# Kernel optimization log

Measured on AMD Instinct MI355X. Metric: run time of the kernel, lower is better.

## Reference

```python
import jax, jax.numpy as jnp
import numpy as np

WIN = 9
WIN_SIZE = float(WIN ** 3)
LBD = 1.0
EPS = 1e-5


def _box_sum(x, win=WIN):
    """Separable sum over a win^3 window with zero padding == conv3d with all-ones kernel."""
    pad = win // 2
    for ax in (2, 3, 4):  # spatial axes of [N, C, H, W, D]
        wd = [1] * 5
        wd[ax] = win
        padc = [(0, 0)] * 5
        padc[ax] = (pad, pad)
        x = jax.lax.reduce_window(x, 0.0, jax.lax.add, tuple(wd), (1, 1, 1, 1, 1), padc)
    return x


def _warp3d(images, flows):
    """Trilinear warp. images [B,G,C,H,W,D], flows [B,G,3,H,W,D] (voxel displacements,
    channels ordered as (H, W, D) axes). Border-clamped sampling."""
    B, G, C, H, W, D = images.shape
    N = B * G
    img = images.reshape(N, C, H, W, D)
    flo = flows.reshape(N, 3, H, W, D)
    ft = flo.dtype
    gh = jnp.arange(H, dtype=ft).reshape(H, 1, 1)
    gw = jnp.arange(W, dtype=ft).reshape(1, W, 1)
    gd = jnp.arange(D, dtype=ft).reshape(1, 1, D)
    ch = jnp.clip(flo[:, 0] + gh, 0.0, H - 1.0)
    cw = jnp.clip(flo[:, 1] + gw, 0.0, W - 1.0)
    cd = jnp.clip(flo[:, 2] + gd, 0.0, D - 1.0)
    h0f = jnp.floor(ch); w0f = jnp.floor(cw); d0f = jnp.floor(cd)
    fh = ch - h0f; fw = cw - w0f; fd = cd - d0f
    h0 = h0f.astype(jnp.int32); w0 = w0f.astype(jnp.int32); d0 = d0f.astype(jnp.int32)
    h1 = jnp.minimum(h0 + 1, H - 1)
    w1 = jnp.minimum(w0 + 1, W - 1)
    d1 = jnp.minimum(d0 + 1, D - 1)
    flat = img.reshape(N, C, H * W * D)

    def gather(hi, wi, di):
        lin = ((hi * W + wi) * D + di).reshape(N, 1, H * W * D)
        return jnp.take_along_axis(flat, lin, axis=2).reshape(N, C, H, W, D)

    out = jnp.zeros_like(img)
    for hi, wh in ((h0, 1.0 - fh), (h1, fh)):
        for wi, ww in ((w0, 1.0 - fw), (w1, fw)):
            for di, wdw in ((d0, 1.0 - fd), (d1, fd)):
                w8 = (wh * ww * wdw)[:, None]  # [N,1,H,W,D]
                out = out + w8 * gather(hi, wi, di)
    return out.reshape(B, G, C, H, W, D)


def setup_inputs() -> dict:
    key = jax.random.key(0)
    k1, k2 = jax.random.split(key)
    images = jax.random.normal(k1, (1, 4, 1, 128, 128, 128), dtype=jnp.float32)
    warps = jax.random.normal(k2, (1, 4, 3, 128, 128, 128), dtype=jnp.float32)
    return {"images": images, "warps": warps}


def reference(images, warps):
    B, G, C, H, W, D = images.shape
    warped = _warp3d(images, warps).reshape(B * G, C, H, W, D)
    # groupwise template = mean over the B*G warped volumes, broadcast back
    template = jnp.broadcast_to(jnp.mean(warped, axis=0, keepdims=True), warped.shape)
    Ii, Ji = template, warped
    # 5 stat channels: I, J, I^2, J^2, IJ; groups=5 box-filter conv == per-channel box sum
    stats = jnp.concatenate([Ii, Ji, Ii * Ii, Ji * Ji, Ii * Ji], axis=1)
    sums = _box_sum(stats)
    I_sum, J_sum, I2_sum, J2_sum, IJ_sum = jnp.split(sums, 5, axis=1)
    cross = IJ_sum - J_sum / WIN_SIZE * I_sum
    I_var = I2_sum - I_sum / WIN_SIZE * I_sum
    J_var = J2_sum - J_sum / WIN_SIZE * J_sum
    cc = cross * cross / (I_var * J_var + EPS)
    lncc = -jnp.mean(cc)
    # Grad3d('l2') on warps [B,G,3,H,W,D]: dx over H (axis 3), dy over W (axis 4), dz over D (axis 5)
    dx = jnp.square(warps[:, :, :, 1:] - warps[:, :, :, :-1])
    dy = jnp.square(warps[:, :, :, :, 1:] - warps[:, :, :, :, :-1])
    dz = jnp.square(warps[..., 1:] - warps[..., :-1])
    g2 = (jnp.mean(dx) + jnp.mean(dy) + jnp.mean(dz)) / 3.0
    return lncc + LBD * g2
```

## Files before the change

### kernel.cpp

```cpp
#include <hip/hip_runtime.h>
#include <hip/hip_bf16.h>


#define NVOX (128*128*128)
#define NGRP 4
#define NCH 14

__global__ __launch_bounds__(256) void k_pack(const float* __restrict__ img,
                                              float4* __restrict__ P4)
{
    int idx = blockIdx.x * 256 + threadIdx.x;
    int v = idx & (NVOX - 1);
    int g = idx >> 21;
    int d = v & 127;
    int w = (v >> 7) & 127;
    const float* im = img + (size_t)g * NVOX;
    int vd1 = (d < 127) ? v + 1 : v;
    int vw1 = (w < 127) ? v + 128 : v;
    int vw1d1 = (d < 127) ? vw1 + 1 : vw1;
    P4[idx] = make_float4(im[v], im[vd1], im[vw1], im[vw1d1]);
}

__global__ __launch_bounds__(256) void k_warp_stats_p4(
    const float4* __restrict__ P4, const float* __restrict__ flo,
    float* __restrict__ S, double* __restrict__ pg2)
{
    __shared__ float jt[NGRP][256];
    int t = threadIdx.x;
    int v = blockIdx.x * 256 + t;
    int d = v & 127;
    int w = (v >> 7) & 127;
    int h = v >> 14;
    float g2s = 0.f;

#pragma unroll
    for (int g = 0; g < NGRP; ++g) {
        const float* f = flo + (size_t)g * 3 * NVOX;
        float fx = f[v], fy = f[NVOX + v], fz = f[2 * NVOX + v];
        if (h < 127) {
            float a = f[v + 16384] - fx;
            float b = f[NVOX + v + 16384] - fy;
            float c = f[2 * NVOX + v + 16384] - fz;
            g2s += a * a + b * b + c * c;
        }
        if (w < 127) {
            float a = f[v + 128] - fx;
            float b = f[NVOX + v + 128] - fy;
            float c = f[2 * NVOX + v + 128] - fz;
            g2s += a * a + b * b + c * c;
        }
        if (d < 127) {
            float a = f[v + 1] - fx;
            float b = f[NVOX + v + 1] - fy;
            float c = f[2 * NVOX + v + 1] - fz;
            g2s += a * a + b * b + c * c;
        }
        float ch = fminf(fmaxf(fx + (float)h, 0.f), 127.f);
        float cw = fminf(fmaxf(fy + (float)w, 0.f), 127.f);
        float cd = fminf(fmaxf(fz + (float)d, 0.f), 127.f);
        float h0f = floorf(ch), w0f = floorf(cw), d0f = floorf(cd);
        int h0 = (int)h0f, w0 = (int)w0f, d0 = (int)d0f;
        float fh = ch - h0f, fw = cw - w0f, fd = cd - d0f;
        int h1 = min(h0 + 1, 127);
        const float4* P = P4 + (size_t)g * NVOX;
        float4 q0 = P[h0 * 16384 + w0 * 128 + d0];
        float4 q1 = P[h1 * 16384 + w0 * 128 + d0];
        float c00 = q0.x + fd * (q0.y - q0.x);
        float c01 = q0.z + fd * (q0.w - q0.z);
        float c10 = q1.x + fd * (q1.y - q1.x);
        float c11 = q1.z + fd * (q1.w - q1.z);
        float c0 = c00 + fw * (c01 - c00);
        float c1 = c10 + fw * (c11 - c10);
        jt[g][t] = c0 + fh * (c1 - c0);
    }
    __syncthreads();

    float s[NCH];
#pragma unroll
    for (int c = 0; c < NCH; ++c) s[c] = 0.f;
    int lbase = t & 128;
#pragma unroll
    for (int k = -4; k <= 4; ++k) {
        int q = d + k;
        if ((unsigned)q < 128u) {
            int tq = lbase + q;
            float j0 = jt[0][tq], j1 = jt[1][tq], j2 = jt[2][tq], j3 = jt[3][tq];
            float tm = 0.25f * (j0 + j1 + j2 + j3);
            s[0] += tm;       s[1] += tm * tm;
            s[2] += j0;  s[3] += j0 * j0;  s[4]  += tm * j0;
            s[5] += j1;  s[6] += j1 * j1;  s[7]  += tm * j1;
            s[8] += j2;  s[9] += j2 * j2;  s[10] += tm * j2;
            s[11] += j3; s[12] += j3 * j3; s[13] += tm * j3;
        }
    }
#pragma unroll
    for (int c = 0; c < NCH; ++c) S[(size_t)c * NVOX + v] = s[c];

    double val = (double)g2s;
    for (int off = 32; off; off >>= 1) val += __shfl_down(val, off, 64);
    __shared__ double wsum[4];
    int lane = t & 63, wid = t >> 6;
    if (lane == 0) wsum[wid] = val;
    __syncthreads();
    if (t == 0) pg2[blockIdx.x] = wsum[0] + wsum[1] + wsum[2] + wsum[3];
}

__global__ __launch_bounds__(256) void k_warp_stats_direct(
    const float* __restrict__ img, const float* __restrict__ flo,
    float* __restrict__ S, double* __restrict__ pg2)
{
    __shared__ float jt[NGRP][256];
    int t = threadIdx.x;
    int v = blockIdx.x * 256 + t;
    int d = v & 127;
    int w = (v >> 7) & 127;
    int h = v >> 14;
    float g2s = 0.f;

#pragma unroll
    for (int g = 0; g < NGRP; ++g) {
        const float* f = flo + (size_t)g * 3 * NVOX;
        float fx = f[v], fy = f[NVOX + v], fz = f[2 * NVOX + v];
        if (h < 127) {
            float a = f[v + 16384] - fx;
            float b = f[NVOX + v + 16384] - fy;
            float c = f[2 * NVOX + v + 16384] - fz;
            g2s += a * a + b * b + c * c;
        }
        if (w < 127) {
            float a = f[v + 128] - fx;
            float b = f[NVOX + v + 128] - fy;
            float c = f[2 * NVOX + v + 128] - fz;
            g2s += a * a + b * b + c * c;
        }
        if (d < 127) {
            float a = f[v + 1] - fx;
            float b = f[NVOX + v + 1] - fy;
            float c = f[2 * NVOX + v + 1] - fz;
            g2s += a * a + b * b + c * c;
        }
        float ch = fminf(fmaxf(fx + (float)h, 0.f), 127.f);
        float cw = fminf(fmaxf(fy + (float)w, 0.f), 127.f);
        float cd = fminf(fmaxf(fz + (float)d, 0.f), 127.f);
        float h0f = floorf(ch), w0f = floorf(cw), d0f = floorf(cd);
        int h0 = (int)h0f, w0 = (int)w0f, d0 = (int)d0f;
        float fh = ch - h0f, fw = cw - w0f, fd = cd - d0f;
        int h1 = min(h0 + 1, 127), w1 = min(w0 + 1, 127), d1 = min(d0 + 1, 127);
        const float* im = img + (size_t)g * NVOX;
        int b00 = (h0 * 128 + w0) * 128;
        int b01 = (h0 * 128 + w1) * 128;
        int b10 = (h1 * 128 + w0) * 128;
        int b11 = (h1 * 128 + w1) * 128;
        float v000 = im[b00 + d0], v001 = im[b00 + d1];
        float v010 = im[b01 + d0], v011 = im[b01 + d1];
        float v100 = im[b10 + d0], v101 = im[b10 + d1];
        float v110 = im[b11 + d0], v111 = im[b11 + d1];
        float c00 = v000 + fd * (v001 - v000);
        float c01 = v010 + fd * (v011 - v010);
        float c10 = v100 + fd * (v101 - v100);
        float c11 = v110 + fd * (v111 - v110);
        float c0 = c00 + fw * (c01 - c00);
        float c1 = c10 + fw * (c11 - c10);
        jt[g][t] = c0 + fh * (c1 - c0);
    }
    __syncthreads();

    float s[NCH];
#pragma unroll
    for (int c = 0; c < NCH; ++c) s[c] = 0.f;
    int lbase = t & 128;
#pragma unroll
    for (int k = -4; k <= 4; ++k) {
        int q = d + k;
        if ((unsigned)q < 128u) {
            int tq = lbase + q;
            float j0 = jt[0][tq], j1 = jt[1][tq], j2 = jt[2][tq], j3 = jt[3][tq];
            float tm = 0.25f * (j0 + j1 + j2 + j3);
            s[0] += tm;       s[1] += tm * tm;
            s[2] += j0;  s[3] += j0 * j0;  s[4]  += tm * j0;
            s[5] += j1;  s[6] += j1 * j1;  s[7]  += tm * j1;
            s[8] += j2;  s[9] += j2 * j2;  s[10] += tm * j2;
            s[11] += j3; s[12] += j3 * j3; s[13] += tm * j3;
        }
    }
#pragma unroll
    for (int c = 0; c < NCH; ++c) S[(size_t)c * NVOX + v] = s[c];

    double val = (double)g2s;
    for (int off = 32; off; off >>= 1) val += __shfl_down(val, off, 64);
    __shared__ double wsum[4];
    int lane = t & 63, wid = t >> 6;
    if (lane == 0) wsum[wid] = val;
    __syncthreads();
    if (t == 0) pg2[blockIdx.x] = wsum[0] + wsum[1] + wsum[2] + wsum[3];
}

__global__ __launch_bounds__(256) void k_sum_w(float* __restrict__ S)
{
    __shared__ float tile[128 * 64];
    int t = threadIdx.x;
    int bid = blockIdx.x;
    int half = bid & 1;
    int chh = bid >> 1;
    size_t base = (size_t)chh * 16384 + half * 64;
#pragma unroll
    for (int it = 0; it < 8; ++it) {
        int idx4 = it * 256 + t;
        int w = idx4 >> 4, dq = idx4 & 15;
        *(float4*)(tile + w * 64 + dq * 4) =
            *(const float4*)(S + base + (size_t)w * 128 + dq * 4);
    }
    __syncthreads();
    int dq = t & 15;
    int wq = t >> 4;
    int w0 = wq * 8;
    float4 s = make_float4(0.f, 0.f, 0.f, 0.f);
#pragma unroll
    for (int k = -4; k <= 4; ++k) {
        int q = w0 + k;
        if ((unsigned)q < 128u) {
            float4 tv = *(const float4*)(tile + q * 64 + dq * 4);
            s.x += tv.x; s.y += tv.y; s.z += tv.z; s.w += tv.w;
        }
    }
    *(float4*)(S + base + (size_t)w0 * 128 + dq * 4) = s;
#pragma unroll
    for (int wi = 1; wi < 8; ++wi) {
        int w = w0 + wi;
        int qa = w + 4;
        if (qa < 128) {
            float4 tv = *(const float4*)(tile + qa * 64 + dq * 4);
            s.x += tv.x; s.y += tv.y; s.z += tv.z; s.w += tv.w;
        }
        int qr = w - 5;
        if (qr >= 0) {
            float4 tv = *(const float4*)(tile + qr * 64 + dq * 4);
            s.x -= tv.x; s.y -= tv.y; s.z -= tv.z; s.w -= tv.w;
        }
        *(float4*)(S + base + (size_t)w * 128 + dq * 4) = s;
    }
}

__device__ __forceinline__ float cc4(float4 I, float4 I2, float4 J, float4 J2, float4 IJ)
{
    const float inv = 1.0f / 729.0f;
    float r = 0.f;
    {
        float cr = IJ.x - J.x * I.x * inv, iv = I2.x - I.x * I.x * inv, jv = J2.x - J.x * J.x * inv;
        r += cr * cr / (iv * jv + 1e-5f);
    }
    {
        float cr = IJ.y - J.y * I.y * inv, iv = I2.y - I.y * I.y * inv, jv = J2.y - J.y * J.y * inv;
        r += cr * cr / (iv * jv + 1e-5f);
    }
    {
        float cr = IJ.z - J.z * I.z * inv, iv = I2.z - I.z * I.z * inv, jv = J2.z - J.z * J.z * inv;
        r += cr * cr / (iv * jv + 1e-5f);
    }
    {
        float cr = IJ.w - J.w * I.w * inv, iv = I2.w - I.w * I.w * inv, jv = J2.w - J.w * J.w * inv;
        r += cr * cr / (iv * jv + 1e-5f);
    }
    return r;
}

#define LOADH(c, a0, a1)                                                       \
    do {                                                                       \
        const float* cp = S + (size_t)(c) * NVOX + cbase;                      \
        _Pragma("unroll")                                                      \
        for (int it = 0; it < 3; ++it) {                                       \
            int idx = it * 256 + t;                                            \
            if (idx < 640) {                           \
                int row = idx >> 4, dqu = idx & 15;                            \
                int rr = r0 + row;                                             \
                float4 vv = make_float4(0.f, 0.f, 0.f, 0.f);                   \
                if ((unsigned)rr < 128u)                                       \
                    vv = *(const float4*)(cp + (size_t)rr * 16384 + dqu * 4);  \
                int la = row * 65 + dqu * 4;                                   \
                tile[la] = vv.x; tile[la + 1] = vv.y;                          \
                tile[la + 2] = vv.z; tile[la + 3] = vv.w;                      \
            }                                                                  \
        }                                                                      \
        __syncthreads();                                                       \
        {                                                                      \
            int hl = hg * 2;                                                   \
            float4 sum = make_float4(0.f, 0.f, 0.f, 0.f);                      \
            _Pragma("unroll")                                                  \
            for (int k = 0; k < 9; ++k) {                                      \
                const float* tp = tile + (hl + k) * 65 + dq * 4;               \
                sum.x += tp[0]; sum.y += tp[1]; sum.z += tp[2]; sum.w += tp[3];\
            }                                                                  \
            a0 = sum;                                                          \
            const float* ta = tile + (hl + 9) * 65 + dq * 4;                   \
            const float* tr = tile + hl * 65 + dq * 4;                         \
            sum.x += ta[0] - tr[0]; sum.y += ta[1] - tr[1];                    \
            sum.z += ta[2] - tr[2]; sum.w += ta[3] - tr[3];                    \
            a1 = sum;                                                          \
        }                                                                      \
        __syncthreads();                                                       \
    } while (0)

__global__ __launch_bounds__(256) void k_sum_h_cc(const float* __restrict__ S,
                                                  double* __restrict__ pcc)
{
    __shared__ float tile[40 * 65];
    int t = threadIdx.x;
    int bid = blockIdx.x;
    int dh = bid & 1;
    int hq = (bid >> 1) & 3;
    int w = bid >> 3;
    int r0 = hq * 32 - 4;
    size_t cbase = (size_t)w * 128 + dh * 64;
    int dq = t & 15;
    int hg = t >> 4;

    float4 Ia0, Ia1, I2a0, I2a1, Ja0, Ja1, J2a0, J2a1, IJa0, IJa1;
    float lsum = 0.f;

    LOADH(0, Ia0, Ia1);
    LOADH(1, I2a0, I2a1);
    for (int g = 0; g < NGRP; ++g) {
        LOADH(2 + 3 * g, Ja0, Ja1);
        LOADH(3 + 3 * g, J2a0, J2a1);
        LOADH(4 + 3 * g, IJa0, IJa1);
        lsum += cc4(Ia0, I2a0, Ja0, J2a0, IJa0);
        lsum += cc4(Ia1, I2a1, Ja1, J2a1, IJa1);
    }

    double val = (double)lsum;
    for (int off = 32; off; off >>= 1) val += __shfl_down(val, off, 64);
    __shared__ double wsum[4];
    int lane = t & 63, wid = t >> 6;
    if (lane == 0) wsum[wid] = val;
    __syncthreads();
    if (t == 0) pcc[bid] = wsum[0] + wsum[1] + wsum[2] + wsum[3];
}

__global__ __launch_bounds__(256) void k_finalize(const double* __restrict__ pg2,
                                                  const double* __restrict__ pcc,
                                                  float* __restrict__ out)
{
    double s_cc = 0.0, s_g2 = 0.0;
    for (int i = threadIdx.x; i < 1024; i += 256) s_cc += pcc[i];
    for (int i = threadIdx.x; i < 8192; i += 256) s_g2 += pg2[i];
    for (int off = 32; off; off >>= 1) {
        s_cc += __shfl_down(s_cc, off, 64);
        s_g2 += __shfl_down(s_g2, off, 64);
    }
    __shared__ double a[4], b[4];
    int lane = threadIdx.x & 63, wid = threadIdx.x >> 6;
    if (lane == 0) { a[wid] = s_cc; b[wid] = s_g2; }
    __syncthreads();
    if (threadIdx.x == 0) {
        double cc_sum = a[0] + a[1] + a[2] + a[3];
        double g2_sum = b[0] + b[1] + b[2] + b[3];
        double lncc = -cc_sum / (4.0 * (double)NVOX);
        double g2 = g2_sum / (3.0 * 12.0 * 127.0 * 128.0 * 128.0);
        out[0] = (float)(lncc + g2);
    }
}

extern "C" void kernel_launch(void* const* d_in, const int* in_sizes, int n_in,
                              void* d_out, int out_size, void* d_ws, size_t ws_size,
                              hipStream_t stream)
{
    const float* img = (const float*)d_in[0];
    const float* flo = (const float*)d_in[1];
    float* out = (float*)d_out;

    const size_t S_BYTES  = (size_t)NCH * NVOX * 4;
    const size_t P4_BYTES = (size_t)NGRP * NVOX * 16;
    float* S = (float*)d_ws;

    if (ws_size >= S_BYTES + P4_BYTES + 8192 * 8 + 1024 * 8) {
        float4* P4 = (float4*)((char*)d_ws + S_BYTES);
        double* pg2 = (double*)((char*)d_ws + S_BYTES + P4_BYTES);
        double* pcc = pg2 + 8192;
        k_pack<<<(NGRP * NVOX) / 256, 256, 0, stream>>>(img, P4);
        k_warp_stats_p4<<<NVOX / 256, 256, 0, stream>>>(P4, flo, S, pg2);
        k_sum_w<<<NCH * 128 * 2, 256, 0, stream>>>(S);
        k_sum_h_cc<<<1024, 256, 0, stream>>>(S, pcc);
        k_finalize<<<1, 256, 0, stream>>>(pg2, pcc, out);
    } else {
        double* pg2 = (double*)((char*)d_ws + S_BYTES);
        double* pcc = pg2 + 8192;
        k_warp_stats_direct<<<NVOX / 256, 256, 0, stream>>>(img, flo, S, pg2);
        k_sum_w<<<NCH * 128 * 2, 256, 0, stream>>>(S);
        k_sum_h_cc<<<1024, 256, 0, stream>>>(S, pcc);
        k_finalize<<<1, 256, 0, stream>>>(pg2, pcc, out);
    }
}
```

Measured before the change: 394.0 us.

## Drop packed-neighbor pass, split direct warp into swizzled launches, pad shared tile

Removes the k_pack pre-pass and the float4 neighbor buffer, so the warp kernel always gathers eight corners straight from the image. The warp/stats kernel is split into four launches of 2048 blocks each, with the block index swizzled across the H dimension. This is likely meant to spread concurrently running blocks across varied regions and improve L2 locality of the random gathers. The k_sum_w shared tile row stride is padded from 64 to 68 floats to reduce LDS bank conflicts. It trades the extra pack pass and its memory traffic for eight scalar gathers per voxel instead of two float4 loads, and adds launch overhead.

```diff
diff --git a/kernel.cpp b/kernel.cpp
--- a/kernel.cpp
+++ b/kernel.cpp
@@ -6,28 +6,14 @@
 #define NGRP 4
 #define NCH 14
 
-__global__ __launch_bounds__(256) void k_pack(const float* __restrict__ img,
-                                              float4* __restrict__ P4)
-{
-    int idx = blockIdx.x * 256 + threadIdx.x;
-    int v = idx & (NVOX - 1);
-    int g = idx >> 21;
-    int d = v & 127;
-    int w = (v >> 7) & 127;
-    const float* im = img + (size_t)g * NVOX;
-    int vd1 = (d < 127) ? v + 1 : v;
-    int vw1 = (w < 127) ? v + 128 : v;
-    int vw1d1 = (d < 127) ? vw1 + 1 : vw1;
-    P4[idx] = make_float4(im[v], im[vd1], im[vw1], im[vw1d1]);
-}
-
-__global__ __launch_bounds__(256) void k_warp_stats_p4(
-    const float4* __restrict__ P4, const float* __restrict__ flo,
-    float* __restrict__ S, double* __restrict__ pg2)
+__global__ __launch_bounds__(256) void k_warp_stats_d(
+    const float* __restrict__ img, const float* __restrict__ flo,
+    float* __restrict__ S, double* __restrict__ pg2, int blk0)
 {
     __shared__ float jt[NGRP][256];
     int t = threadIdx.x;
-    int v = blockIdx.x * 256 + t;
+    int b = blk0 + ((blockIdx.x & 7) << 8) + (blockIdx.x >> 3);
+    int v = b * 256 + t;
     int d = v & 127;
     int w = (v >> 7) & 127;
     int h = v >> 14;
@@ -39,105 +25,21 @@
         float fx = f[v], fy = f[NVOX + v], fz = f[2 * NVOX + v];
         if (h < 127) {
             float a = f[v + 16384] - fx;
-            float b = f[NVOX + v + 16384] - fy;
+            float bb = f[NVOX + v + 16384] - fy;
             float c = f[2 * NVOX + v + 16384] - fz;
-            g2s += a * a + b * b + c * c;
+            g2s += a * a + bb * bb + c * c;
         }
         if (w < 127) {
             float a = f[v + 128] - fx;
-            float b = f[NVOX + v + 128] - fy;
+            float bb = f[NVOX + v + 128] - fy;
             float c = f[2 * NVOX + v + 128] - fz;
-            g2s += a * a + b * b + c * c;
+            g2s += a * a + bb * bb + c * c;
         }
         if (d < 127) {
             float a = f[v + 1] - fx;
-            float b = f[NVOX + v + 1] - fy;
+            float bb = f[NVOX + v + 1] - fy;
             float c = f[2 * NVOX + v + 1] - fz;
-            g2s += a * a + b * b + c * c;
-        }
-        float ch = fminf(fmaxf(fx + (float)h, 0.f), 127.f);
-        float cw = fminf(fmaxf(fy + (float)w, 0.f), 127.f);
-        float cd = fminf(fmaxf(fz + (float)d, 0.f), 127.f);
-        float h0f = floorf(ch), w0f = floorf(cw), d0f = floorf(cd);
-        int h0 = (int)h0f, w0 = (int)w0f, d0 = (int)d0f;
-        float fh = ch - h0f, fw = cw - w0f, fd = cd - d0f;
-        int h1 = min(h0 + 1, 127);
-        const float4* P = P4 + (size_t)g * NVOX;
-        float4 q0 = P[h0 * 16384 + w0 * 128 + d0];
-        float4 q1 = P[h1 * 16384 + w0 * 128 + d0];
-        float c00 = q0.x + fd * (q0.y - q0.x);
-        float c01 = q0.z + fd * (q0.w - q0.z);
-        float c10 = q1.x + fd * (q1.y - q1.x);
-        float c11 = q1.z + fd * (q1.w - q1.z);
-        float c0 = c00 + fw * (c01 - c00);
-        float c1 = c10 + fw * (c11 - c10);
-        jt[g][t] = c0 + fh * (c1 - c0);
-    }
-    __syncthreads();
-
-    float s[NCH];
-#pragma unroll
-    for (int c = 0; c < NCH; ++c) s[c] = 0.f;
-    int lbase = t & 128;
-#pragma unroll
-    for (int k = -4; k <= 4; ++k) {
-        int q = d + k;
-        if ((unsigned)q < 128u) {
-            int tq = lbase + q;
-            float j0 = jt[0][tq], j1 = jt[1][tq], j2 = jt[2][tq], j3 = jt[3][tq];
-            float tm = 0.25f * (j0 + j1 + j2 + j3);
-            s[0] += tm;       s[1] += tm * tm;
-            s[2] += j0;  s[3] += j0 * j0;  s[4]  += tm * j0;
-            s[5] += j1;  s[6] += j1 * j1;  s[7]  += tm * j1;
-            s[8] += j2;  s[9] += j2 * j2;  s[10] += tm * j2;
-            s[11] += j3; s[12] += j3 * j3; s[13] += tm * j3;
-        }
-    }
-#pragma unroll
-    for (int c = 0; c < NCH; ++c) S[(size_t)c * NVOX + v] = s[c];
-
-    double val = (double)g2s;
-    for (int off = 32; off; off >>= 1) val += __shfl_down(val, off, 64);
-    __shared__ double wsum[4];
-    int lane = t & 63, wid = t >> 6;
-    if (lane == 0) wsum[wid] = val;
-    __syncthreads();
-    if (t == 0) pg2[blockIdx.x] = wsum[0] + wsum[1] + wsum[2] + wsum[3];
-}
-
-__global__ __launch_bounds__(256) void k_warp_stats_direct(
-    const float* __restrict__ img, const float* __restrict__ flo,
-    float* __restrict__ S, double* __restrict__ pg2)
-{
-    __shared__ float jt[NGRP][256];
-    int t = threadIdx.x;
-    int v = blockIdx.x * 256 + t;
-    int d = v & 127;
-    int w = (v >> 7) & 127;
-    int h = v >> 14;
-    float g2s = 0.f;
-
-#pragma unroll
-    for (int g = 0; g < NGRP; ++g) {
-        const float* f = flo + (size_t)g * 3 * NVOX;
-        float fx = f[v], fy = f[NVOX + v], fz = f[2 * NVOX + v];
-        if (h < 127) {
-            float a = f[v + 16384] - fx;
-            float b = f[NVOX + v + 16384] - fy;
-            float c = f[2 * NVOX + v + 16384] - fz;
-            g2s += a * a + b * b + c * c;
-        }
-        if (w < 127) {
-            float a = f[v + 128] - fx;
-            float b = f[NVOX + v + 128] - fy;
-            float c = f[2 * NVOX + v + 128] - fz;
-            g2s += a * a + b * b + c * c;
-        }
-        if (d < 127) {
-            float a = f[v + 1] - fx;
-            float b = f[NVOX + v + 1] - fy;
-            float c = f[2 * NVOX + v + 1] - fz;
-            g2s += a * a + b * b + c * c;
+            g2s += a * a + bb * bb + c * c;
         }
         float ch = fminf(fmaxf(fx + (float)h, 0.f), 127.f);
         float cw = fminf(fmaxf(fy + (float)w, 0.f), 127.f);
@@ -192,12 +94,12 @@
     int lane = t & 63, wid = t >> 6;
     if (lane == 0) wsum[wid] = val;
     __syncthreads();
-    if (t == 0) pg2[blockIdx.x] = wsum[0] + wsum[1] + wsum[2] + wsum[3];
+    if (t == 0) pg2[b] = wsum[0] + wsum[1] + wsum[2] + wsum[3];
 }
 
 __global__ __launch_bounds__(256) void k_sum_w(float* __restrict__ S)
 {
-    __shared__ float tile[128 * 64];
+    __shared__ float tile[128 * 68];
     int t = threadIdx.x;
     int bid = blockIdx.x;
     int half = bid & 1;
@@ -207,7 +109,7 @@
     for (int it = 0; it < 8; ++it) {
         int idx4 = it * 256 + t;
         int w = idx4 >> 4, dq = idx4 & 15;
-        *(float4*)(tile + w * 64 + dq * 4) =
+        *(float4*)(tile + w * 68 + dq * 4) =
             *(const float4*)(S + base + (size_t)w * 128 + dq * 4);
     }
     __syncthreads();
@@ -219,7 +121,7 @@
     for (int k = -4; k <= 4; ++k) {
         int q = w0 + k;
         if ((unsigned)q < 128u) {
-            float4 tv = *(const float4*)(tile + q * 64 + dq * 4);
+            float4 tv = *(const float4*)(tile + q * 68 + dq * 4);
             s.x += tv.x; s.y += tv.y; s.z += tv.z; s.w += tv.w;
         }
     }
@@ -229,12 +131,12 @@
         int w = w0 + wi;
         int qa = w + 4;
         if (qa < 128) {
-            float4 tv = *(const float4*)(tile + qa * 64 + dq * 4);
+            float4 tv = *(const float4*)(tile + qa * 68 + dq * 4);
             s.x += tv.x; s.y += tv.y; s.z += tv.z; s.w += tv.w;
         }
         int qr = w - 5;
         if (qr >= 0) {
-            float4 tv = *(const float4*)(tile + qr * 64 + dq * 4);
+            float4 tv = *(const float4*)(tile + qr * 68 + dq * 4);
             s.x -= tv.x; s.y -= tv.y; s.z -= tv.z; s.w -= tv.w;
         }
         *(float4*)(S + base + (size_t)w * 128 + dq * 4) = s;
@@ -368,25 +270,16 @@
     const float* flo = (const float*)d_in[1];
     float* out = (float*)d_out;
 
-    const size_t S_BYTES  = (size_t)NCH * NVOX * 4;
-    const size_t P4_BYTES = (size_t)NGRP * NVOX * 16;
+    const size_t S_BYTES = (size_t)NCH * NVOX * 4;
     float* S = (float*)d_ws;
-
-    if (ws_size >= S_BYTES + P4_BYTES + 8192 * 8 + 1024 * 8) {
-        float4* P4 = (float4*)((char*)d_ws + S_BYTES);
-        double* pg2 = (double*)((char*)d_ws + S_BYTES + P4_BYTES);
-        double* pcc = pg2 + 8192;
-        k_pack<<<(NGRP * NVOX) / 256, 256, 0, stream>>>(img, P4);
-        k_warp_stats_p4<<<NVOX / 256, 256, 0, stream>>>(P4, flo, S, pg2);
-        k_sum_w<<<NCH * 128 * 2, 256, 0, stream>>>(S);
-        k_sum_h_cc<<<1024, 256, 0, stream>>>(S, pcc);
-        k_finalize<<<1, 256, 0, stream>>>(pg2, pcc, out);
-    } else {
-        double* pg2 = (double*)((char*)d_ws + S_BYTES);
-        double* pcc = pg2 + 8192;
-        k_warp_stats_direct<<<NVOX / 256, 256, 0, stream>>>(img, flo, S, pg2);
-        k_sum_w<<<NCH * 128 * 2, 256, 0, stream>>>(S);
-        k_sum_h_cc<<<1024, 256, 0, stream>>>(S, pcc);
-        k_finalize<<<1, 256, 0, stream>>>(pg2, pcc, out);
-    }
-}
+    double* pg2 = (double*)((char*)d_ws + S_BYTES);
+    double* pcc = pg2 + 8192;
+
+    k_warp_stats_d<<<2048, 256, 0, stream>>>(img, flo, S, pg2, 0);
+    k_warp_stats_d<<<2048, 256, 0, stream>>>(img, flo, S, pg2, 2048);
+    k_warp_stats_d<<<2048, 256, 0, stream>>>(img, flo, S, pg2, 4096);
+    k_warp_stats_d<<<2048, 256, 0, stream>>>(img, flo, S, pg2, 6144);
+    k_sum_w<<<NCH * 128 * 2, 256, 0, stream>>>(S);
+    k_sum_h_cc<<<1024, 256, 0, stream>>>(S, pcc);
+    k_finalize<<<1, 256, 0, stream>>>(pg2, pcc, out);
+}
```

Result: faster. 351.5 us (-10.8%).
